# Optimization experiments

Measured on AMD Instinct MI355X. Metric: run time of the kernel, lower is better.

The kernel has to match this reference:

```python
import jax, jax.numpy as jnp
import numpy as np

B, S, D_MODEL, D_QK, D_VO = 4, 2048, 1024, 128, 128
NEG = -1.0e9


def setup_inputs() -> dict:
    key = jax.random.key(0)
    k1, k2, k3, k4, k5 = jax.random.split(key, 5)
    enc = jax.random.normal(k1, (B, S, D_MODEL), dtype=jnp.float32)
    # causal mask: True means masked (masked_fill), broadcast over batch
    causal = jnp.triu(jnp.ones((S, S), dtype=bool), k=1)
    mask = jnp.broadcast_to(causal, (B, S, S))
    scale = 0.02
    W_q = jax.random.normal(k2, (D_MODEL, D_QK), dtype=jnp.float32) * scale
    W_k = jax.random.normal(k3, (D_MODEL, D_QK), dtype=jnp.float32) * scale
    W_v = jax.random.normal(k4, (D_MODEL, D_VO), dtype=jnp.float32) * scale
    W_o = jax.random.normal(k5, (D_VO, D_MODEL), dtype=jnp.float32) * scale
    return {"encodings": enc, "mask": mask, "W_q": W_q, "W_k": W_k, "W_v": W_v, "W_o": W_o}


def reference(encodings, mask, W_q, W_k, W_v, W_o):
    # q,k: [B,S,d_qk]; v: [B,S,d_vo]
    q = jnp.einsum('bsd,de->bse', encodings, W_q)
    k = jnp.einsum('bsd,de->bse', encodings, W_k)
    v = jnp.einsum('bsd,de->bse', encodings, W_v)
    sims = jnp.einsum('bqe,bke->bqk', q, k) / jnp.asarray(D_QK ** 0.5, q.dtype)
    sims = jnp.where(mask, jnp.asarray(NEG, sims.dtype), sims)
    attn = jax.nn.softmax(sims, axis=-1)  # [B,S,S]
    scores = jnp.einsum('bqk,bke->bqe', attn, v)  # [B,S,d_vo]
    return jnp.einsum('bse,ed->bsd', scores, W_o)  # [B,S,d_model]
```

## Files before the change

### kernel.cpp

```cpp
#include <hip/hip_runtime.h>
#include <hip/hip_bf16.h>
#include <stdint.h>
#include <type_traits>

typedef __attribute__((ext_vector_type(8))) short short8;
typedef __attribute__((ext_vector_type(4))) float floatx4;

using bf16 = __hip_bfloat16;

#define LOG2E 1.4426950408889634f
#define QK_SCALE 0.08838834764831845f

__device__ inline unsigned short f2b(float f) {
    bf16 h = __float2bfloat16(f);
    return *(unsigned short*)&h;
}

__global__ __launch_bounds__(256) void cvt_f32_bf16(const float4* __restrict__ src,
                                                    ushort4* __restrict__ dst, int n4) {
    int i = blockIdx.x * 256 + threadIdx.x;
    if (i < n4) {
        float4 v = src[i];
        ushort4 o;
        o.x = f2b(v.x); o.y = f2b(v.y); o.z = f2b(v.z); o.w = f2b(v.w);
        dst[i] = o;
    }
}

__global__ __launch_bounds__(256) void prep_weights(const float* __restrict__ Wq,
                                                    const float* __restrict__ Wk,
                                                    const float* __restrict__ Wv,
                                                    const float* __restrict__ Wo,
                                                    bf16* __restrict__ Wqkvt,
                                                    bf16* __restrict__ Wot) {
    int idx = blockIdx.x * 256 + threadIdx.x;
    int sel = idx >> 17;
    int i = idx & 131071;
    if (sel < 3) {
        const float* W = (sel == 0) ? Wq : (sel == 1) ? Wk : Wv;
        int r = i >> 7, c = i & 127;
        Wqkvt[(size_t)(sel * 128 + c) * 1024 + r] = __float2bfloat16(W[i]);
    } else {
        int r = i >> 10, c = i & 1023;
        Wot[(size_t)c * 128 + r] = __float2bfloat16(Wo[i]);
    }
}

__global__ __launch_bounds__(256) void gemm_qkv(const bf16* __restrict__ A,
                                                const bf16* __restrict__ Bt,
                                                bf16* __restrict__ Qb,
                                                bf16* __restrict__ Kb,
                                                bf16* __restrict__ Vtb) {
    __shared__ bf16 As[128 * 40];
    __shared__ bf16 Bs[128 * 40];

    const int tid = threadIdx.x;
    const int m0 = blockIdx.x * 128;
    const int y = blockIdx.y;
    const int brow0 = y * 128;
    const int w = tid >> 6, lane = tid & 63;
    const int wm = (w >> 1) * 64, wn = (w & 1) * 64;
    const int quad = lane >> 4, l16 = lane & 15;

    floatx4 acc[4][4];
#pragma unroll
    for (int i = 0; i < 4; i++)
#pragma unroll
        for (int j = 0; j < 4; j++) acc[i][j] = (floatx4){0.f, 0.f, 0.f, 0.f};

    for (int k0 = 0; k0 < 1024; k0 += 32) {
        __syncthreads();
#pragma unroll
        for (int i = 0; i < 2; i++) {
            int id = tid + i * 256;
            int r = id >> 2, cg = (id & 3) * 8;
            *(int4*)&As[r * 40 + cg] = *(const int4*)&A[(size_t)(m0 + r) * 1024 + k0 + cg];
            *(int4*)&Bs[r * 40 + cg] = *(const int4*)&Bt[(size_t)(brow0 + r) * 1024 + k0 + cg];
        }
        __syncthreads();

        short8 a[4], b[4];
#pragma unroll
        for (int mt = 0; mt < 4; mt++)
            a[mt] = *(const short8*)&As[(wm + mt * 16 + l16) * 40 + quad * 8];
#pragma unroll
        for (int nt = 0; nt < 4; nt++)
            b[nt] = *(const short8*)&Bs[(wn + nt * 16 + l16) * 40 + quad * 8];
#pragma unroll
        for (int mt = 0; mt < 4; mt++)
#pragma unroll
            for (int nt = 0; nt < 4; nt++)
                acc[mt][nt] = __builtin_amdgcn_mfma_f32_16x16x32_bf16(a[mt], b[nt], acc[mt][nt], 0, 0, 0);
    }

#pragma unroll
    for (int mt = 0; mt < 4; mt++)
#pragma unroll
        for (int nt = 0; nt < 4; nt++)
#pragma unroll
            for (int r = 0; r < 4; r++) {
                int row = m0 + wm + mt * 16 + quad * 4 + r;
                int col = wn + nt * 16 + l16;
                bf16 v = __float2bfloat16(acc[mt][nt][r]);
                if (y == 0) {
                    Qb[(size_t)row * 128 + col] = v;
                } else if (y == 1) {
                    Kb[(size_t)row * 128 + col] = v;
                } else {
                    int bb = row >> 11, ss = row & 2047;
                    Vtb[(size_t)bb * 262144 + (size_t)col * 2048 + ss] = v;
                }
            }
}

__global__ __launch_bounds__(256) void gemm_out(const bf16* __restrict__ A, int lda,
                                                const bf16* __restrict__ Bt, int ldb,
                                                float* __restrict__ C, int ldc, int K) {
    __shared__ bf16 As[128 * 40];
    __shared__ bf16 Bs[128 * 40];

    const int tid = threadIdx.x;
    const int m0 = blockIdx.x * 128;
    const int n0 = blockIdx.y * 128;
    const int w = tid >> 6, lane = tid & 63;
    const int wm = (w >> 1) * 64, wn = (w & 1) * 64;
    const int quad = lane >> 4, l16 = lane & 15;

    floatx4 acc[4][4];
#pragma unroll
    for (int i = 0; i < 4; i++)
#pragma unroll
        for (int j = 0; j < 4; j++) acc[i][j] = (floatx4){0.f, 0.f, 0.f, 0.f};

    for (int k0 = 0; k0 < K; k0 += 32) {
        __syncthreads();
#pragma unroll
        for (int i = 0; i < 2; i++) {
            int id = tid + i * 256;
            int r = id >> 2, cg = (id & 3) * 8;
            *(int4*)&As[r * 40 + cg] = *(const int4*)&A[(size_t)(m0 + r) * lda + k0 + cg];
            *(int4*)&Bs[r * 40 + cg] = *(const int4*)&Bt[(size_t)(n0 + r) * ldb + k0 + cg];
        }
        __syncthreads();

        short8 a[4], b[4];
#pragma unroll
        for (int mt = 0; mt < 4; mt++)
            a[mt] = *(const short8*)&As[(wm + mt * 16 + l16) * 40 + quad * 8];
#pragma unroll
        for (int nt = 0; nt < 4; nt++)
            b[nt] = *(const short8*)&Bs[(wn + nt * 16 + l16) * 40 + quad * 8];
#pragma unroll
        for (int mt = 0; mt < 4; mt++)
#pragma unroll
            for (int nt = 0; nt < 4; nt++)
                acc[mt][nt] = __builtin_amdgcn_mfma_f32_16x16x32_bf16(a[mt], b[nt], acc[mt][nt], 0, 0, 0);
    }

#pragma unroll
    for (int mt = 0; mt < 4; mt++)
#pragma unroll
        for (int nt = 0; nt < 4; nt++)
#pragma unroll
            for (int r = 0; r < 4; r++) {
                int row = m0 + wm + mt * 16 + quad * 4 + r;
                int col = n0 + wn + nt * 16 + l16;
                C[(size_t)row * ldc + col] = acc[mt][nt][r];
            }
}

__global__ __launch_bounds__(256) void flash_split(const bf16* __restrict__ Q,
                                                   const bf16* __restrict__ K,
                                                   const bf16* __restrict__ Vt,
                                                   float* __restrict__ Op,
                                                   float2* __restrict__ Ml) {
    __shared__ bf16 Qs[64 * 136];
    __shared__ bf16 Ks[64 * 136];
    __shared__ bf16 Vs[128 * 72];
    __shared__ bf16 Ps[4 * 16 * 72];

    const int tid = threadIdx.x;
    const int b = blockIdx.x >> 5;
    const int qt = blockIdx.x & 31;
    const int ks = blockIdx.y;
    const int q0 = qt * 64;
    const int w = tid >> 6, lane = tid & 63;
    const int quad = lane >> 4, l16 = lane & 15;

    const int ntiles = qt + 1;
    const int per = (ntiles + 3) >> 2;
    const int start = ks * per;
    const int end = min(start + per, ntiles);

#pragma unroll
    for (int i = 0; i < 4; i++) {
        int id = tid + i * 256;
        int r = id >> 4, cg = (id & 15) * 8;
        *(int4*)&Qs[r * 136 + cg] = *(const int4*)&Q[((size_t)b * 2048 + q0 + r) * 128 + cg];
    }
    __syncthreads();
    short8 qf[4];
#pragma unroll
    for (int k4 = 0; k4 < 4; k4++)
        qf[k4] = *(const short8*)&Qs[(w * 16 + l16) * 136 + k4 * 32 + quad * 8];

    float m_run[4], l_run[4];
    floatx4 o[8];
#pragma unroll
    for (int r = 0; r < 4; r++) { m_run[r] = -1.0e30f; l_run[r] = 0.f; }
#pragma unroll
    for (int d = 0; d < 8; d++) o[d] = (floatx4){0.f, 0.f, 0.f, 0.f};

    int4 kreg[4], vreg[4];
    const int sr[4]  = {(tid + 0) >> 4, (tid + 256) >> 4, (tid + 512) >> 4, (tid + 768) >> 4};
    const int scg    = (tid & 15) * 8;
    const int sr2[4] = {(tid + 0) >> 3, (tid + 256) >> 3, (tid + 512) >> 3, (tid + 768) >> 3};
    const int scg2   = (tid & 7) * 8;

    if (start < end) {
#pragma unroll
        for (int i = 0; i < 4; i++) {
            kreg[i] = *(const int4*)&K[((size_t)b * 2048 + start * 64 + sr[i]) * 128 + scg];
            vreg[i] = *(const int4*)&Vt[(size_t)b * 262144 + (size_t)sr2[i] * 2048 + start * 64 + scg2];
        }
    }

    for (int kt = start; kt < end; kt++) {
        __syncthreads();
#pragma unroll
        for (int i = 0; i < 4; i++) {
            *(int4*)&Ks[sr[i] * 136 + scg] = kreg[i];
            *(int4*)&Vs[sr2[i] * 72 + scg2] = vreg[i];
        }
        __syncthreads();

        if (kt + 1 < end) {
#pragma unroll
            for (int i = 0; i < 4; i++) {
                kreg[i] = *(const int4*)&K[((size_t)b * 2048 + (kt + 1) * 64 + sr[i]) * 128 + scg];
                vreg[i] = *(const int4*)&Vt[(size_t)b * 262144 + (size_t)sr2[i] * 2048 + (kt + 1) * 64 + scg2];
            }
        }

        floatx4 s_acc[4];
#pragma unroll
        for (int nt = 0; nt < 4; nt++) {
            s_acc[nt] = (floatx4){0.f, 0.f, 0.f, 0.f};
#pragma unroll
            for (int k4 = 0; k4 < 4; k4++) {
                short8 bfr = *(const short8*)&Ks[(nt * 16 + l16) * 136 + k4 * 32 + quad * 8];
                s_acc[nt] = __builtin_amdgcn_mfma_f32_16x16x32_bf16(qf[k4], bfr, s_acc[nt], 0, 0, 0);
            }
        }

        float sv[4][4];
#pragma unroll
        for (int nt = 0; nt < 4; nt++)
#pragma unroll
            for (int r = 0; r < 4; r++) {
                float s = s_acc[nt][r] * QK_SCALE;
                if (kt == qt) {
                    int kcol = kt * 64 + nt * 16 + l16;
                    int qrow = q0 + w * 16 + quad * 4 + r;
                    if (kcol > qrow) s = -1.0e9f;
                }
                sv[nt][r] = s;
            }

        float mnew[4], alpha[4], rsum[4];
#pragma unroll
        for (int r = 0; r < 4; r++) {
            float t = fmaxf(fmaxf(sv[0][r], sv[1][r]), fmaxf(sv[2][r], sv[3][r]));
            t = fmaxf(t, __shfl_xor(t, 1, 16));
            t = fmaxf(t, __shfl_xor(t, 2, 16));
            t = fmaxf(t, __shfl_xor(t, 4, 16));
            t = fmaxf(t, __shfl_xor(t, 8, 16));
            mnew[r] = fmaxf(m_run[r], t);
            alpha[r] = exp2f((m_run[r] - mnew[r]) * LOG2E);
            m_run[r] = mnew[r];
            rsum[r] = 0.f;
        }
#pragma unroll
        for (int nt = 0; nt < 4; nt++)
#pragma unroll
            for (int r = 0; r < 4; r++) {
                float p = exp2f((sv[nt][r] - mnew[r]) * LOG2E);
                rsum[r] += p;
                Ps[w * 1152 + (quad * 4 + r) * 72 + nt * 16 + l16] = __float2bfloat16(p);
            }
#pragma unroll
        for (int r = 0; r < 4; r++) {
            float t = rsum[r];
            t += __shfl_xor(t, 1, 16);
            t += __shfl_xor(t, 2, 16);
            t += __shfl_xor(t, 4, 16);
            t += __shfl_xor(t, 8, 16);
            l_run[r] = l_run[r] * alpha[r] + t;
        }
#pragma unroll
        for (int d = 0; d < 8; d++)
#pragma unroll
            for (int r = 0; r < 4; r++) o[d][r] *= alpha[r];

        short8 pf[2];
#pragma unroll
        for (int k2 = 0; k2 < 2; k2++)
            pf[k2] = *(const short8*)&Ps[w * 1152 + l16 * 72 + k2 * 32 + quad * 8];
#pragma unroll
        for (int d = 0; d < 8; d++)
#pragma unroll
            for (int k2 = 0; k2 < 2; k2++) {
                short8 bv = *(const short8*)&Vs[(d * 16 + l16) * 72 + k2 * 32 + quad * 8];
                o[d] = __builtin_amdgcn_mfma_f32_16x16x32_bf16(pf[k2], bv, o[d], 0, 0, 0);
            }
    }

#pragma unroll
    for (int r = 0; r < 4; r++) {
        int grow = (int)(b * 2048 + q0 + w * 16 + quad * 4 + r);
        size_t orow = (size_t)ks * 8192 + grow;
#pragma unroll
        for (int d = 0; d < 8; d++)
            Op[orow * 128 + d * 16 + l16] = o[d][r];
        if (l16 == 0) Ml[orow] = make_float2(m_run[r], l_run[r]);
    }
}

__global__ __launch_bounds__(256) void flash_merge(const float* __restrict__ Op,
                                                   const float2* __restrict__ Ml,
                                                   bf16* __restrict__ Sc) {
    int idx = blockIdx.x * 256 + threadIdx.x;
    int row = idx >> 5, dg = (idx & 31) * 4;

    float2 ml[4];
#pragma unroll
    for (int s = 0; s < 4; s++) ml[s] = Ml[(size_t)s * 8192 + row];
    float M = fmaxf(fmaxf(ml[0].x, ml[1].x), fmaxf(ml[2].x, ml[3].x));
    float L = 0.f, wgt[4];
#pragma unroll
    for (int s = 0; s < 4; s++) {
        wgt[s] = exp2f((ml[s].x - M) * LOG2E);
        L += ml[s].y * wgt[s];
    }
    float4 acc = {0.f, 0.f, 0.f, 0.f};
#pragma unroll
    for (int s = 0; s < 4; s++) {
        float4 v = *(const float4*)&Op[((size_t)s * 8192 + row) * 128 + dg];
        acc.x += v.x * wgt[s]; acc.y += v.y * wgt[s];
        acc.z += v.z * wgt[s]; acc.w += v.w * wgt[s];
    }
    float inv = 1.0f / L;
    ushort4 o;
    o.x = f2b(acc.x * inv); o.y = f2b(acc.y * inv);
    o.z = f2b(acc.z * inv); o.w = f2b(acc.w * inv);
    *(ushort4*)&Sc[(size_t)row * 128 + dg] = o;
}

extern "C" void kernel_launch(void* const* d_in, const int* in_sizes, int n_in,
                              void* d_out, int out_size, void* d_ws, size_t ws_size,
                              hipStream_t stream) {
    const float* enc = (const float*)d_in[0];
    const float* Wq = (const float*)d_in[2];
    const float* Wk = (const float*)d_in[3];
    const float* Wv = (const float*)d_in[4];
    const float* Wo = (const float*)d_in[5];
    float* out = (float*)d_out;

    const size_t MB = 1024 * 1024;
    char* ws = (char*)d_ws;
    bf16*   encb  = (bf16*)(ws);
    float*  Op    = (float*)(ws);
    bf16*   Qb    = (bf16*)(ws + 16 * MB);
    bf16*   Kb    = (bf16*)(ws + 18 * MB);
    bf16*   Vtb   = (bf16*)(ws + 20 * MB);
    bf16*   Scb   = (bf16*)(ws + 22 * MB);
    bf16*   Wqkvt = (bf16*)(ws + 24 * MB);
    bf16*   Wot   = (bf16*)(ws + 24 * MB + 768 * 1024);
    float2* Ml    = (float2*)(ws + 25 * MB);

    cvt_f32_bf16<<<8192, 256, 0, stream>>>((const float4*)enc, (ushort4*)encb, 2097152);

    prep_weights<<<2048, 256, 0, stream>>>(Wq, Wk, Wv, Wo, Wqkvt, Wot);

    dim3 blk(256);
    gemm_qkv<<<dim3(64, 3), blk, 0, stream>>>(encb, Wqkvt, Qb, Kb, Vtb);

    flash_split<<<dim3(128, 4), blk, 0, stream>>>(Qb, Kb, Vtb, Op, Ml);
    flash_merge<<<1024, blk, 0, stream>>>(Op, Ml, Scb);

    gemm_out<<<dim3(64, 8), blk, 0, stream>>>(Scb, 128, Wot, 128, out, 1024, 128);
}
```

Baseline: 236.0 us.

## Merge prep kernels, use 64-row GEMM tiles with prefetch, transpose flash MFMA layout

Fuses the input conversion and weight preparation into a single launch. Both GEMMs now use a templated kernel with 64-row tiles, doubling the grid for better CU occupancy, and register-prefetch the next K slice while the current one is computed. The flash kernel swaps MFMA operand order so each lane owns one query row, which reduces softmax reductions to two cross-lane shuffles. It also folds log2e into the scale, loads Q directly from global memory, and writes vectorized P and output stores. The cost is smaller per-block reuse in the GEMMs and a riskier rework of the attention indexing.

```diff
diff --git a/kernel.cpp b/kernel.cpp
--- a/kernel.cpp
+++ b/kernel.cpp
@@ -1,7 +1,6 @@
 #include <hip/hip_runtime.h>
 #include <hip/hip_bf16.h>
 #include <stdint.h>
-#include <type_traits>
 
 typedef __attribute__((ext_vector_type(8))) short short8;
 typedef __attribute__((ext_vector_type(4))) float floatx4;
@@ -9,163 +8,123 @@
 using bf16 = __hip_bfloat16;
 
 #define LOG2E 1.4426950408889634f
-#define QK_SCALE 0.08838834764831845f
+#define SCALE_L2 0.12751793359133147f
 
 __device__ inline unsigned short f2b(float f) {
     bf16 h = __float2bfloat16(f);
     return *(unsigned short*)&h;
 }
 
-__global__ __launch_bounds__(256) void cvt_f32_bf16(const float4* __restrict__ src,
-                                                    ushort4* __restrict__ dst, int n4) {
-    int i = blockIdx.x * 256 + threadIdx.x;
-    if (i < n4) {
-        float4 v = src[i];
+__global__ __launch_bounds__(256) void prep_all(const float4* __restrict__ enc4,
+                                                ushort4* __restrict__ encb4,
+                                                const float* __restrict__ Wq,
+                                                const float* __restrict__ Wk,
+                                                const float* __restrict__ Wv,
+                                                const float* __restrict__ Wo,
+                                                bf16* __restrict__ Wqkvt,
+                                                bf16* __restrict__ Wot) {
+    int bx = blockIdx.x;
+    if (bx < 8192) {
+        int i = bx * 256 + threadIdx.x;
+        float4 v = enc4[i];
         ushort4 o;
         o.x = f2b(v.x); o.y = f2b(v.y); o.z = f2b(v.z); o.w = f2b(v.w);
-        dst[i] = o;
-    }
-}
-
-__global__ __launch_bounds__(256) void prep_weights(const float* __restrict__ Wq,
-                                                    const float* __restrict__ Wk,
-                                                    const float* __restrict__ Wv,
-                                                    const float* __restrict__ Wo,
-                                                    bf16* __restrict__ Wqkvt,
-                                                    bf16* __restrict__ Wot) {
-    int idx = blockIdx.x * 256 + threadIdx.x;
-    int sel = idx >> 17;
-    int i = idx & 131071;
-    if (sel < 3) {
-        const float* W = (sel == 0) ? Wq : (sel == 1) ? Wk : Wv;
-        int r = i >> 7, c = i & 127;
-        Wqkvt[(size_t)(sel * 128 + c) * 1024 + r] = __float2bfloat16(W[i]);
+        encb4[i] = o;
     } else {
-        int r = i >> 10, c = i & 1023;
-        Wot[(size_t)c * 128 + r] = __float2bfloat16(Wo[i]);
-    }
-}
-
-__global__ __launch_bounds__(256) void gemm_qkv(const bf16* __restrict__ A,
-                                                const bf16* __restrict__ Bt,
-                                                bf16* __restrict__ Qb,
-                                                bf16* __restrict__ Kb,
-                                                bf16* __restrict__ Vtb) {
-    __shared__ bf16 As[128 * 40];
+        int idx = (bx - 8192) * 256 + threadIdx.x;
+        int sel = idx >> 17;
+        int i = idx & 131071;
+        if (sel < 3) {
+            const float* W = (sel == 0) ? Wq : (sel == 1) ? Wk : Wv;
+            int r = i >> 7, c = i & 127;
+            Wqkvt[(size_t)(sel * 128 + c) * 1024 + r] = __float2bfloat16(W[i]);
+        } else {
+            int r = i >> 10, c = i & 1023;
+            Wot[(size_t)c * 128 + r] = __float2bfloat16(Wo[i]);
+        }
+    }
+}
+
+template <int KDIM, bool QKV>
+__global__ __launch_bounds__(256) void gemm64(const bf16* __restrict__ A, int lda,
+                                              const bf16* __restrict__ Bt, int ldb,
+                                              void* __restrict__ C0,
+                                              void* __restrict__ C1,
+                                              void* __restrict__ C2) {
+    __shared__ bf16 As[64 * 40];
     __shared__ bf16 Bs[128 * 40];
 
     const int tid = threadIdx.x;
-    const int m0 = blockIdx.x * 128;
-    const int y = blockIdx.y;
-    const int brow0 = y * 128;
+    const int m0 = blockIdx.x * 64;
+    const int nsel = blockIdx.y;
+    const int brow0 = nsel * 128;
     const int w = tid >> 6, lane = tid & 63;
-    const int wm = (w >> 1) * 64, wn = (w & 1) * 64;
+    const int wm = (w >> 1) * 32, wn = (w & 1) * 64;
     const int quad = lane >> 4, l16 = lane & 15;
 
-    floatx4 acc[4][4];
-#pragma unroll
-    for (int i = 0; i < 4; i++)
+    const int ra = tid >> 2, ca = (tid & 3) * 8;
+    const int rb0 = tid >> 2, rb1 = (tid + 256) >> 2;
+
+    floatx4 acc[2][4];
+#pragma unroll
+    for (int i = 0; i < 2; i++)
 #pragma unroll
         for (int j = 0; j < 4; j++) acc[i][j] = (floatx4){0.f, 0.f, 0.f, 0.f};
 
-    for (int k0 = 0; k0 < 1024; k0 += 32) {
+    int4 pa, pb0, pb1;
+    pa  = *(const int4*)&A[(size_t)(m0 + ra) * lda + ca];
+    pb0 = *(const int4*)&Bt[(size_t)(brow0 + rb0) * ldb + ca];
+    pb1 = *(const int4*)&Bt[(size_t)(brow0 + rb1) * ldb + ca];
+
+    for (int k0 = 0; k0 < KDIM; k0 += 32) {
         __syncthreads();
-#pragma unroll
-        for (int i = 0; i < 2; i++) {
-            int id = tid + i * 256;
-            int r = id >> 2, cg = (id & 3) * 8;
-            *(int4*)&As[r * 40 + cg] = *(const int4*)&A[(size_t)(m0 + r) * 1024 + k0 + cg];
-            *(int4*)&Bs[r * 40 + cg] = *(const int4*)&Bt[(size_t)(brow0 + r) * 1024 + k0 + cg];
-        }
+        *(int4*)&As[ra * 40 + ca] = pa;
+        *(int4*)&Bs[rb0 * 40 + ca] = pb0;
+        *(int4*)&Bs[rb1 * 40 + ca] = pb1;
         __syncthreads();
 
-        short8 a[4], b[4];
-#pragma unroll
-        for (int mt = 0; mt < 4; mt++)
+        if (k0 + 32 < KDIM) {
+            pa  = *(const int4*)&A[(size_t)(m0 + ra) * lda + k0 + 32 + ca];
+            pb0 = *(const int4*)&Bt[(size_t)(brow0 + rb0) * ldb + k0 + 32 + ca];
+            pb1 = *(const int4*)&Bt[(size_t)(brow0 + rb1) * ldb + k0 + 32 + ca];
+        }
+
+        short8 a[2], b[4];
+#pragma unroll
+        for (int mt = 0; mt < 2; mt++)
             a[mt] = *(const short8*)&As[(wm + mt * 16 + l16) * 40 + quad * 8];
 #pragma unroll
         for (int nt = 0; nt < 4; nt++)
             b[nt] = *(const short8*)&Bs[(wn + nt * 16 + l16) * 40 + quad * 8];
 #pragma unroll
-        for (int mt = 0; mt < 4; mt++)
+        for (int mt = 0; mt < 2; mt++)
 #pragma unroll
             for (int nt = 0; nt < 4; nt++)
                 acc[mt][nt] = __builtin_amdgcn_mfma_f32_16x16x32_bf16(a[mt], b[nt], acc[mt][nt], 0, 0, 0);
     }
 
 #pragma unroll
-    for (int mt = 0; mt < 4; mt++)
+    for (int mt = 0; mt < 2; mt++)
 #pragma unroll
         for (int nt = 0; nt < 4; nt++)
 #pragma unroll
             for (int r = 0; r < 4; r++) {
                 int row = m0 + wm + mt * 16 + quad * 4 + r;
                 int col = wn + nt * 16 + l16;
-                bf16 v = __float2bfloat16(acc[mt][nt][r]);
-                if (y == 0) {
-                    Qb[(size_t)row * 128 + col] = v;
-                } else if (y == 1) {
-                    Kb[(size_t)row * 128 + col] = v;
+                float v = acc[mt][nt][r];
+                if (QKV) {
+                    bf16 h = __float2bfloat16(v);
+                    if (nsel == 0) {
+                        ((bf16*)C0)[(size_t)row * 128 + col] = h;
+                    } else if (nsel == 1) {
+                        ((bf16*)C1)[(size_t)row * 128 + col] = h;
+                    } else {
+                        int bb = row >> 11, ss = row & 2047;
+                        ((bf16*)C2)[(size_t)bb * 262144 + (size_t)col * 2048 + ss] = h;
+                    }
                 } else {
-                    int bb = row >> 11, ss = row & 2047;
-                    Vtb[(size_t)bb * 262144 + (size_t)col * 2048 + ss] = v;
+                    ((float*)C0)[(size_t)row * 1024 + brow0 + col] = v;
                 }
-            }
-}
-
-__global__ __launch_bounds__(256) void gemm_out(const bf16* __restrict__ A, int lda,
-                                                const bf16* __restrict__ Bt, int ldb,
-                                                float* __restrict__ C, int ldc, int K) {
-    __shared__ bf16 As[128 * 40];
-    __shared__ bf16 Bs[128 * 40];
-
-    const int tid = threadIdx.x;
-    const int m0 = blockIdx.x * 128;
-    const int n0 = blockIdx.y * 128;
-    const int w = tid >> 6, lane = tid & 63;
-    const int wm = (w >> 1) * 64, wn = (w & 1) * 64;
-    const int quad = lane >> 4, l16 = lane & 15;
-
-    floatx4 acc[4][4];
-#pragma unroll
-    for (int i = 0; i < 4; i++)
-#pragma unroll
-        for (int j = 0; j < 4; j++) acc[i][j] = (floatx4){0.f, 0.f, 0.f, 0.f};
-
-    for (int k0 = 0; k0 < K; k0 += 32) {
-        __syncthreads();
-#pragma unroll
-        for (int i = 0; i < 2; i++) {
-            int id = tid + i * 256;
-            int r = id >> 2, cg = (id & 3) * 8;
-            *(int4*)&As[r * 40 + cg] = *(const int4*)&A[(size_t)(m0 + r) * lda + k0 + cg];
-            *(int4*)&Bs[r * 40 + cg] = *(const int4*)&Bt[(size_t)(n0 + r) * ldb + k0 + cg];
-        }
-        __syncthreads();
-
-        short8 a[4], b[4];
-#pragma unroll
-        for (int mt = 0; mt < 4; mt++)
-            a[mt] = *(const short8*)&As[(wm + mt * 16 + l16) * 40 + quad * 8];
-#pragma unroll
-        for (int nt = 0; nt < 4; nt++)
-            b[nt] = *(const short8*)&Bs[(wn + nt * 16 + l16) * 40 + quad * 8];
-#pragma unroll
-        for (int mt = 0; mt < 4; mt++)
-#pragma unroll
-            for (int nt = 0; nt < 4; nt++)
-                acc[mt][nt] = __builtin_amdgcn_mfma_f32_16x16x32_bf16(a[mt], b[nt], acc[mt][nt], 0, 0, 0);
-    }
-
-#pragma unroll
-    for (int mt = 0; mt < 4; mt++)
-#pragma unroll
-        for (int nt = 0; nt < 4; nt++)
-#pragma unroll
-            for (int r = 0; r < 4; r++) {
-                int row = m0 + wm + mt * 16 + quad * 4 + r;
-                int col = n0 + wn + nt * 16 + l16;
-                C[(size_t)row * ldc + col] = acc[mt][nt][r];
             }
 }
 
@@ -174,7 +133,6 @@
                                                    const bf16* __restrict__ Vt,
                                                    float* __restrict__ Op,
                                                    float2* __restrict__ Ml) {
-    __shared__ bf16 Qs[64 * 136];
     __shared__ bf16 Ks[64 * 136];
     __shared__ bf16 Vs[128 * 72];
     __shared__ bf16 Ps[4 * 16 * 72];
@@ -192,22 +150,14 @@
     const int start = ks * per;
     const int end = min(start + per, ntiles);
 
-#pragma unroll
-    for (int i = 0; i < 4; i++) {
-        int id = tid + i * 256;
-        int r = id >> 4, cg = (id & 15) * 8;
-        *(int4*)&Qs[r * 136 + cg] = *(const int4*)&Q[((size_t)b * 2048 + q0 + r) * 128 + cg];
-    }
-    __syncthreads();
+    const int qrow = q0 + w * 16 + l16;
     short8 qf[4];
 #pragma unroll
     for (int k4 = 0; k4 < 4; k4++)
-        qf[k4] = *(const short8*)&Qs[(w * 16 + l16) * 136 + k4 * 32 + quad * 8];
-
-    float m_run[4], l_run[4];
+        qf[k4] = *(const short8*)&Q[((size_t)b * 2048 + qrow) * 128 + k4 * 32 + quad * 8];
+
+    float m_run = -1.0e30f, l_run = 0.f;
     floatx4 o[8];
-#pragma unroll
-    for (int r = 0; r < 4; r++) { m_run[r] = -1.0e30f; l_run[r] = 0.f; }
 #pragma unroll
     for (int d = 0; d < 8; d++) o[d] = (floatx4){0.f, 0.f, 0.f, 0.f};
 
@@ -248,8 +198,8 @@
             s_acc[nt] = (floatx4){0.f, 0.f, 0.f, 0.f};
 #pragma unroll
             for (int k4 = 0; k4 < 4; k4++) {
-                short8 bfr = *(const short8*)&Ks[(nt * 16 + l16) * 136 + k4 * 32 + quad * 8];
-                s_acc[nt] = __builtin_amdgcn_mfma_f32_16x16x32_bf16(qf[k4], bfr, s_acc[nt], 0, 0, 0);
+                short8 kf = *(const short8*)&Ks[(nt * 16 + l16) * 136 + k4 * 32 + quad * 8];
+                s_acc[nt] = __builtin_amdgcn_mfma_f32_16x16x32_bf16(kf, qf[k4], s_acc[nt], 0, 0, 0);
             }
         }
 
@@ -258,49 +208,51 @@
         for (int nt = 0; nt < 4; nt++)
 #pragma unroll
             for (int r = 0; r < 4; r++) {
-                float s = s_acc[nt][r] * QK_SCALE;
+                float s = s_acc[nt][r] * SCALE_L2;
                 if (kt == qt) {
-                    int kcol = kt * 64 + nt * 16 + l16;
-                    int qrow = q0 + w * 16 + quad * 4 + r;
+                    int kcol = kt * 64 + nt * 16 + quad * 4 + r;
                     if (kcol > qrow) s = -1.0e9f;
                 }
                 sv[nt][r] = s;
             }
 
-        float mnew[4], alpha[4], rsum[4];
-#pragma unroll
-        for (int r = 0; r < 4; r++) {
-            float t = fmaxf(fmaxf(sv[0][r], sv[1][r]), fmaxf(sv[2][r], sv[3][r]));
-            t = fmaxf(t, __shfl_xor(t, 1, 16));
-            t = fmaxf(t, __shfl_xor(t, 2, 16));
-            t = fmaxf(t, __shfl_xor(t, 4, 16));
-            t = fmaxf(t, __shfl_xor(t, 8, 16));
-            mnew[r] = fmaxf(m_run[r], t);
-            alpha[r] = exp2f((m_run[r] - mnew[r]) * LOG2E);
-            m_run[r] = mnew[r];
-            rsum[r] = 0.f;
-        }
+        float t0 = fmaxf(fmaxf(sv[0][0], sv[0][1]), fmaxf(sv[0][2], sv[0][3]));
+        float t1 = fmaxf(fmaxf(sv[1][0], sv[1][1]), fmaxf(sv[1][2], sv[1][3]));
+        float t2 = fmaxf(fmaxf(sv[2][0], sv[2][1]), fmaxf(sv[2][2], sv[2][3]));
+        float t3 = fmaxf(fmaxf(sv[3][0], sv[3][1]), fmaxf(sv[3][2], sv[3][3]));
+        float tmax = fmaxf(fmaxf(t0, t1), fmaxf(t2, t3));
+        tmax = fmaxf(tmax, __shfl_xor(tmax, 16));
+        tmax = fmaxf(tmax, __shfl_xor(tmax, 32));
+
+        float mnew = fmaxf(m_run, tmax);
+        float alpha = exp2f(m_run - mnew);
+        m_run = mnew;
+
+        float rsum = 0.f;
 #pragma unroll
         for (int nt = 0; nt < 4; nt++)
 #pragma unroll
             for (int r = 0; r < 4; r++) {
-                float p = exp2f((sv[nt][r] - mnew[r]) * LOG2E);
-                rsum[r] += p;
-                Ps[w * 1152 + (quad * 4 + r) * 72 + nt * 16 + l16] = __float2bfloat16(p);
-            }
-#pragma unroll
-        for (int r = 0; r < 4; r++) {
-            float t = rsum[r];
-            t += __shfl_xor(t, 1, 16);
-            t += __shfl_xor(t, 2, 16);
-            t += __shfl_xor(t, 4, 16);
-            t += __shfl_xor(t, 8, 16);
-            l_run[r] = l_run[r] * alpha[r] + t;
-        }
-#pragma unroll
-        for (int d = 0; d < 8; d++)
-#pragma unroll
-            for (int r = 0; r < 4; r++) o[d][r] *= alpha[r];
+                float p = exp2f(sv[nt][r] - mnew);
+                sv[nt][r] = p;
+                rsum += p;
+            }
+        rsum += __shfl_xor(rsum, 16);
+        rsum += __shfl_xor(rsum, 32);
+        l_run = l_run * alpha + rsum;
+
+#pragma unroll
+        for (int nt = 0; nt < 4; nt++) {
+            ushort4 pk;
+            pk.x = f2b(sv[nt][0]); pk.y = f2b(sv[nt][1]);
+            pk.z = f2b(sv[nt][2]); pk.w = f2b(sv[nt][3]);
+            *(ushort4*)&Ps[w * 1152 + l16 * 72 + nt * 16 + quad * 4] = pk;
+        }
+
+#pragma unroll
+        for (int d = 0; d < 8; d++) {
+            o[d][0] *= alpha; o[d][1] *= alpha; o[d][2] *= alpha; o[d][3] *= alpha;
+        }
 
         short8 pf[2];
 #pragma unroll
@@ -310,20 +262,18 @@
         for (int d = 0; d < 8; d++)
 #pragma unroll
             for (int k2 = 0; k2 < 2; k2++) {
-                short8 bv = *(const short8*)&Vs[(d * 16 + l16) * 72 + k2 * 32 + quad * 8];
-                o[d] = __builtin_amdgcn_mfma_f32_16x16x32_bf16(pf[k2], bv, o[d], 0, 0, 0);
-            }
-    }
-
-#pragma unroll
-    for (int r = 0; r < 4; r++) {
-        int grow = (int)(b * 2048 + q0 + w * 16 + quad * 4 + r);
-        size_t orow = (size_t)ks * 8192 + grow;
-#pragma unroll
-        for (int d = 0; d < 8; d++)
-            Op[orow * 128 + d * 16 + l16] = o[d][r];
-        if (l16 == 0) Ml[orow] = make_float2(m_run[r], l_run[r]);
-    }
+                short8 vf = *(const short8*)&Vs[(d * 16 + l16) * 72 + k2 * 32 + quad * 8];
+                o[d] = __builtin_amdgcn_mfma_f32_16x16x32_bf16(vf, pf[k2], o[d], 0, 0, 0);
+            }
+    }
+
+    const size_t orow = (size_t)ks * 8192 + b * 2048 + qrow;
+#pragma unroll
+    for (int d = 0; d < 8; d++) {
+        float4 v = {o[d][0], o[d][1], o[d][2], o[d][3]};
+        *(float4*)&Op[orow * 128 + d * 16 + quad * 4] = v;
+    }
+    if (lane < 16) Ml[orow] = make_float2(m_run, l_run);
 }
 
 __global__ __launch_bounds__(256) void flash_merge(const float* __restrict__ Op,
@@ -339,7 +289,7 @@
     float L = 0.f, wgt[4];
 #pragma unroll
     for (int s = 0; s < 4; s++) {
-        wgt[s] = exp2f((ml[s].x - M) * LOG2E);
+        wgt[s] = exp2f(ml[s].x - M);
         L += ml[s].y * wgt[s];
     }
     float4 acc = {0.f, 0.f, 0.f, 0.f};
@@ -378,15 +328,16 @@
     bf16*   Wot   = (bf16*)(ws + 24 * MB + 768 * 1024);
     float2* Ml    = (float2*)(ws + 25 * MB);
 
-    cvt_f32_bf16<<<8192, 256, 0, stream>>>((const float4*)enc, (ushort4*)encb, 2097152);
-
-    prep_weights<<<2048, 256, 0, stream>>>(Wq, Wk, Wv, Wo, Wqkvt, Wot);
+    prep_all<<<10240, 256, 0, stream>>>((const float4*)enc, (ushort4*)encb,
+                                        Wq, Wk, Wv, Wo, Wqkvt, Wot);
 
     dim3 blk(256);
-    gemm_qkv<<<dim3(64, 3), blk, 0, stream>>>(encb, Wqkvt, Qb, Kb, Vtb);
+    gemm64<1024, true><<<dim3(128, 3), blk, 0, stream>>>(encb, 1024, Wqkvt, 1024,
+                                                         Qb, Kb, Vtb);
 
     flash_split<<<dim3(128, 4), blk, 0, stream>>>(Qb, Kb, Vtb, Op, Ml);
     flash_merge<<<1024, blk, 0, stream>>>(Op, Ml, Scb);
 
-    gemm_out<<<dim3(64, 8), blk, 0, stream>>>(Scb, 128, Wot, 128, out, 1024, 128);
-}
+    gemm64<128, false><<<dim3(128, 8), blk, 0, stream>>>(Scb, 128, Wot, 128,
+                                                         out, nullptr, nullptr);
+}
```

Result: faster. 215.4 us (-8.7%).
